# Kernel optimization log

Measured on AMD Instinct MI355X. Metric: run time of the kernel, lower is better.

Reference implementation:

```python
import jax, jax.numpy as jnp
import numpy as np

H_IMG, W_IMG = 160, 160
C1, C2, HEADS, NHOPS = 128, 256, 8, 2
N_NODES = H_IMG * W_IMG


def build_edges(H, W):
    # 3x3 neighborhood (excl. self) + skip edges (i+2,j),(i,j+2); self loops added once
    node = (np.arange(H)[:, None] * W + np.arange(W)[None, :])
    offsets = [(di, dj) for di in (-1, 0, 1) for dj in (-1, 0, 1) if (di, dj) != (0, 0)] + [(2, 0), (0, 2)]
    srcs, dsts = [], []
    for di, dj in offsets:
        i0, i1 = max(0, -di), H - max(0, di)
        j0, j1 = max(0, -dj), W - max(0, dj)
        srcs.append(node[i0:i1, j0:j1].ravel())
        dsts.append(node[i0 + di:i1 + di, j0 + dj:j1 + dj].ravel())
    n = np.arange(H * W)
    srcs.append(n); dsts.append(n)
    return (np.concatenate(srcs).astype(np.int32), np.concatenate(dsts).astype(np.int32))


def setup_inputs() -> dict:
    key = jax.random.key(0)
    ks = jax.random.split(key, 16)
    s = 0.05
    src_np, dst_np = build_edges(H_IMG, W_IMG)
    d = C2 // HEADS
    return {
        "x": jax.random.normal(ks[0], (1, C1, H_IMG, W_IMG), jnp.float32),
        "w_id": jax.random.normal(ks[1], (C2, C1), jnp.float32) * s,
        "w_in": jax.random.normal(ks[2], (C2, C1), jnp.float32) * s,
        "w_gat": jax.random.normal(ks[3], (NHOPS, C2, C2), jnp.float32) * s,
        "a_src": jax.random.normal(ks[4], (NHOPS, HEADS, d), jnp.float32) * s,
        "a_dst": jax.random.normal(ks[5], (NHOPS, HEADS, d), jnp.float32) * s,
        "gat_bias": jax.random.normal(ks[6], (NHOPS, C2), jnp.float32) * s,
        "bn_gamma": jax.random.uniform(ks[7], (NHOPS, C2), jnp.float32, 0.5, 1.5),
        "bn_beta": jax.random.normal(ks[8], (NHOPS, C2), jnp.float32) * s,
        "bn_mean": jax.random.normal(ks[9], (NHOPS, C2), jnp.float32) * s,
        "bn_var": jax.random.uniform(ks[10], (NHOPS, C2), jnp.float32, 0.5, 1.5),
        "w_out": jax.random.normal(ks[11], (C2, C2), jnp.float32) * s,
        "se_w1": jax.random.normal(ks[12], (C2 // 4, C2), jnp.float32) * s,
        "se_b1": jax.random.normal(ks[13], (C2 // 4,), jnp.float32) * s,
        "se_w2": jax.random.normal(ks[14], (C2, C2 // 4), jnp.float32) * s,
        "se_b2": jax.random.normal(ks[15], (C2,), jnp.float32) * s,
        "src": jnp.asarray(src_np),
        "dst": jnp.asarray(dst_np),
    }


def _gat(x, W, a_s, a_d, b, src, dst, N):
    heads, d = a_s.shape
    h = (x @ W.T).reshape(N, heads, d)                      # [N,H,D]
    al_s = jnp.einsum('nhd,hd->nh', h, a_s)                 # [N,H]
    al_d = jnp.einsum('nhd,hd->nh', h, a_d)
    e = jax.nn.leaky_relu(al_s[src] + al_d[dst], 0.2)       # [E,H]
    emax = jax.lax.stop_gradient(jax.ops.segment_max(e, dst, num_segments=N))
    ee = jnp.exp(e - emax[dst])
    denom = jax.ops.segment_sum(ee, dst, num_segments=N)
    alpha = ee / (denom[dst] + 1e-16)                       # segment softmax over incoming edges
    out = jax.ops.segment_sum(h[src] * alpha[..., None], dst, num_segments=N)
    return out.reshape(N, heads * d) + b


def _forward(x, w_id, w_in, w_gat, a_src, a_dst, gat_bias, bn_gamma, bn_beta,
             bn_mean, bn_var, w_out, se_w1, se_b1, se_w2, se_b2, src, dst):
    identity = jnp.einsum('bchw,oc->bohw', x, w_id)
    h = jnp.einsum('bchw,oc->bohw', x, w_in)
    B, C, H, W = h.shape
    N = B * H * W
    xf = h.transpose(0, 2, 3, 1).reshape(N, C)
    for l in range(NHOPS):
        res = xf
        g = _gat(xf, w_gat[l], a_src[l], a_dst[l], gat_bias[l], src, dst, N)
        g = (g - bn_mean[l]) * (bn_gamma[l] * jax.lax.rsqrt(bn_var[l] + 1e-5)) + bn_beta[l]
        xf = jax.nn.relu(g) + res
    y = xf.reshape(B, H, W, C).transpose(0, 3, 1, 2)
    y = jnp.einsum('bchw,oc->bohw', y, w_out)
    # SE block
    w = y.mean(axis=(2, 3))                                 # [B,C]
    w = jax.nn.relu(w @ se_w1.T + se_b1)
    w = jax.nn.sigmoid(w @ se_w2.T + se_b2)
    y = y * w[:, :, None, None]
    return y + identity


def reference(x, w_id, w_in, w_gat, a_src, a_dst, gat_bias, bn_gamma, bn_beta,
              bn_mean, bn_var, w_out, se_w1, se_b1, se_w2, se_b2, src, dst):
    return _forward(x, w_id, w_in, w_gat, a_src, a_dst, gat_bias, bn_gamma, bn_beta,
                    bn_mean, bn_var, w_out, se_w1, se_b1, se_w2, se_b2, src, dst)
```

## Files before the change

### kernel.cpp

```cpp
#include <hip/hip_runtime.h>

#define NN 25600
#define HH 160
#define WW 160
#define C2 256
#define MSLOTS 64

#define B_WIN   0
#define B_WID   32768
#define B_WGAT  65536
#define B_WOUT  196608
#define B_WEND  262144

#define C_BNA   0
#define C_BNB   512
#define C_ASRC  1024
#define C_ADST  1536
#define C_SEW1  2048
#define C_SEB1  18432
#define C_SEW2  18496
#define C_SEB2  34880
#define C_END   35136

typedef __attribute__((ext_vector_type(8))) short bfrag;
typedef __attribute__((ext_vector_type(4))) float ffrag;

__device__ __forceinline__ float b2f(unsigned short u) {
    union { unsigned int ui; float f; } v; v.ui = ((unsigned int)u) << 16; return v.f;
}
__device__ __forceinline__ unsigned short f2b(float f) {
    union { float f; unsigned int u; } v; v.f = f;
    unsigned int u = v.u;
    unsigned int r = (u + 0x7FFFu + ((u >> 16) & 1u)) >> 16;
    return (unsigned short)r;
}
__device__ __forceinline__ float lo16f(unsigned int w) {
    union { unsigned int ui; float f; } v; v.ui = w << 16; return v.f;
}
__device__ __forceinline__ float hi16f(unsigned int w) {
    union { unsigned int ui; float f; } v; v.ui = w & 0xFFFF0000u; return v.f;
}
__device__ __forceinline__ bool probe_f32(const unsigned short* __restrict__ x) {
    int l = threadIdx.x & 63;
    bool wild = false;
#pragma unroll
    for (int i = 0; i < 8; ++i) {
        float v = b2f(x[l * 8 + i]);
        wild |= !(fabsf(v) < 1e6f);
    }
    return __any(wild);
}
__device__ __forceinline__ float ldf(const void* p, long i, bool f32) {
    return f32 ? ((const float*)p)[i] : b2f(((const unsigned short*)p)[i]);
}

__device__ __forceinline__ void gemm_tile_ids(int bid, int& m0, int& o0) {
    int w = (bid & 7) * 200 + (bid >> 3);
    m0 = (w >> 2) * 64;
    o0 = (w & 3) * 64;
}

__device__ __forceinline__ const bfrag* fragp(const unsigned short* buf, int row, int c8) {
    return (const bfrag*)(buf + row * 64 + ((c8 ^ (row & 7)) << 3));
}

__global__ __launch_bounds__(256) void prep_kernel(
    const unsigned short* __restrict__ xp,
    const void* pwin, const void* pwid, const void* pwgat, const void* pwout,
    const void* pasrc, const void* padst, const void* pgbias,
    const void* pbng, const void* pbnb, const void* pbnm, const void* pbnv,
    const void* psew1, const void* pseb1, const void* psew2, const void* pseb2,
    unsigned short* __restrict__ wb, float* __restrict__ cvt,
    float* __restrict__ means, unsigned short* __restrict__ xT)
{
    __shared__ unsigned short T[16 * 136];
    const bool f32 = probe_f32(xp);
    const int tid = threadIdx.x;
    const int bid = blockIdx.x;
    const int gid = bid * 256 + tid;
    const int stride = gridDim.x * 256;

    for (int i = gid; i < MSLOTS * 256; i += stride) means[i] = 0.f;

    for (int i = gid; i < B_WEND; i += stride) {
        const void* s; int o;
        if      (i < B_WID)   { s = pwin;  o = i - B_WIN; }
        else if (i < B_WGAT)  { s = pwid;  o = i - B_WID; }
        else if (i < B_WOUT)  { s = pwgat; o = i - B_WGAT; }
        else                  { s = pwout; o = i - B_WOUT; }
        wb[i] = f32 ? f2b(((const float*)s)[o]) : ((const unsigned short*)s)[o];
    }
    for (int i = gid; i < 512; i += stride) {
        float sc = ldf(pbng, i, f32) * rsqrtf(ldf(pbnv, i, f32) + 1e-5f);
        cvt[C_BNA + i] = sc;
        cvt[C_BNB + i] = (ldf(pgbias, i, f32) - ldf(pbnm, i, f32)) * sc + ldf(pbnb, i, f32);
        cvt[C_ASRC + i] = ldf(pasrc, i, f32);
        cvt[C_ADST + i] = ldf(padst, i, f32);
    }
    for (int i = gid; i < 16384; i += stride) {
        cvt[C_SEW1 + i] = ldf(psew1, i, f32);
        cvt[C_SEW2 + i] = ldf(psew2, i, f32);
    }
    for (int i = gid; i < 64; i += stride)  cvt[C_SEB1 + i] = ldf(pseb1, i, f32);
    for (int i = gid; i < 256; i += stride) cvt[C_SEB2 + i] = ldf(pseb2, i, f32);

    {
        const int n0 = bid * 16;
        const int nl = tid & 15;
        const int cb = tid >> 4;
#pragma unroll
        for (int i = 0; i < 8; ++i) {
            int c = i * 16 + cb;
            long idx = (long)c * NN + n0 + nl;
            T[nl * 136 + c] = f32 ? f2b(((const float*)xp)[idx]) : xp[idx];
        }
        __syncthreads();
        {
            int n = tid >> 4, c0 = (tid & 15) * 8;
            uint4 v = *(const uint4*)&T[n * 136 + c0];
            *(uint4*)(xT + (long)(n0 + n) * 128 + c0) = v;
        }
    }
}

struct SmemC64 { unsigned short Cs[64 * 72]; };
struct SmemGd  { unsigned short As[2][4096], Bs[2][4096]; };
union  SmemNd  { SmemGd g; SmemC64 c; };
struct SmemT   { float T[64 * 73]; };
union  SmemFd  { SmemGd g; SmemT t; };

#define STAGE_TILE(DST, SRC, ROW0, LDA, K0)                                       \
    {                                                                             \
        _Pragma("unroll")                                                         \
        for (int ii = 0; ii < 2; ++ii) {                                          \
            int e = tid + ii * 256;                                               \
            int row = e >> 3;                                                     \
            int q = (e & 7) ^ (row & 7);                                          \
            __builtin_amdgcn_global_load_lds(                                     \
                (const unsigned int*)((SRC) + (long)((ROW0) + row) * (LDA) + (K0) + q * 8), \
                (unsigned int*)&(DST)[e * 8], 16, 0, 0);                          \
        }                                                                         \
    }

__global__ __launch_bounds__(256) void mfma_gemm_kernel(
    const unsigned short* __restrict__ A16,
    const unsigned short* __restrict__ Wi16,
    unsigned short* __restrict__ xf16)
{
    __shared__ SmemNd sm;
    const int tid = threadIdx.x;
    int m0, o0; gemm_tile_ids(blockIdx.x, m0, o0);
    const int lane = tid & 63, wv = tid >> 6;
    const int wm = wv >> 1, wn = wv & 1;
    const int lr = lane & 15, quad = lane >> 4;

    ffrag ai[2][2];
#pragma unroll
    for (int mt = 0; mt < 2; ++mt)
#pragma unroll
        for (int nt = 0; nt < 2; ++nt) ai[mt][nt] = (ffrag){0,0,0,0};

    STAGE_TILE(sm.g.As[0], A16,  m0, 128, 0)
    STAGE_TILE(sm.g.Bs[0], Wi16, o0, 128, 0)
    __syncthreads();
    int cur = 0;
#pragma unroll
    for (int s = 0; s < 2; ++s) {
        if (s == 0) {
            STAGE_TILE(sm.g.As[1], A16,  m0, 128, 64)
            STAGE_TILE(sm.g.Bs[1], Wi16, o0, 128, 64)
        }
#pragma unroll
        for (int ks = 0; ks < 2; ++ks) {
            bfrag a[2], bi[2];
#pragma unroll
            for (int mt = 0; mt < 2; ++mt)
                a[mt] = *fragp(sm.g.As[cur], wm * 32 + mt * 16 + lr, ks * 4 + quad);
#pragma unroll
            for (int nt = 0; nt < 2; ++nt)
                bi[nt] = *fragp(sm.g.Bs[cur], wn * 32 + nt * 16 + lr, ks * 4 + quad);
#pragma unroll
            for (int mt = 0; mt < 2; ++mt)
#pragma unroll
                for (int nt = 0; nt < 2; ++nt)
                    ai[mt][nt] = __builtin_amdgcn_mfma_f32_16x16x32_bf16(a[mt], bi[nt], ai[mt][nt], 0, 0, 0);
        }
        __syncthreads();
        cur ^= 1;
    }
#pragma unroll
    for (int mt = 0; mt < 2; ++mt)
#pragma unroll
        for (int nt = 0; nt < 2; ++nt)
#pragma unroll
            for (int r = 0; r < 4; ++r)
                sm.c.Cs[(wm * 32 + mt * 16 + quad * 4 + r) * 72 + wn * 32 + nt * 16 + lr] = f2b(ai[mt][nt][r]);
    __syncthreads();
#pragma unroll
    for (int it = 0; it < 2; ++it) {
        int e = it * 256 + tid;
        int row = e >> 3, c8 = (e & 7) * 8;
        *(uint4*)(xf16 + (long)(m0 + row) * C2 + o0 + c8) = *(const uint4*)&sm.c.Cs[row * 72 + c8];
    }
}

__global__ __launch_bounds__(256) void gat_gemm_kernel(
    const unsigned short* __restrict__ A16,
    const unsigned short* __restrict__ W16,
    unsigned short* __restrict__ Cout,
    const float* __restrict__ asrc, const float* __restrict__ adst,
    float* __restrict__ als_out, float* __restrict__ ald_out)
{
    __shared__ SmemNd sm;
    const int tid = threadIdx.x;
    int m0, o0; gemm_tile_ids(blockIdx.x, m0, o0);
    const int lane = tid & 63, wv = tid >> 6;
    const int wm = wv >> 1, wn = wv & 1;
    const int lr = lane & 15, quad = lane >> 4;

    ffrag acc[2][2];
#pragma unroll
    for (int mt = 0; mt < 2; ++mt)
#pragma unroll
        for (int nt = 0; nt < 2; ++nt) acc[mt][nt] = (ffrag){0,0,0,0};

    STAGE_TILE(sm.g.As[0], A16, m0, C2, 0)
    STAGE_TILE(sm.g.Bs[0], W16, o0, C2, 0)
    __syncthreads();
    int cur = 0;
#pragma unroll
    for (int s = 0; s < 4; ++s) {
        if (s < 3) {
            STAGE_TILE(sm.g.As[cur ^ 1], A16, m0, C2, (s + 1) * 64)
            STAGE_TILE(sm.g.Bs[cur ^ 1], W16, o0, C2, (s + 1) * 64)
        }
#pragma unroll
        for (int ks = 0; ks < 2; ++ks) {
            bfrag a[2], b[2];
#pragma unroll
            for (int mt = 0; mt < 2; ++mt)
                a[mt] = *fragp(sm.g.As[cur], wm * 32 + mt * 16 + lr, ks * 4 + quad);
#pragma unroll
            for (int nt = 0; nt < 2; ++nt)
                b[nt] = *fragp(sm.g.Bs[cur], wn * 32 + nt * 16 + lr, ks * 4 + quad);
#pragma unroll
            for (int mt = 0; mt < 2; ++mt)
#pragma unroll
                for (int nt = 0; nt < 2; ++nt)
                    acc[mt][nt] = __builtin_amdgcn_mfma_f32_16x16x32_bf16(a[mt], b[nt], acc[mt][nt], 0, 0, 0);
        }
        __syncthreads();
        cur ^= 1;
    }
    {
        const int head = (o0 >> 5) + wn;
        const float as0 = asrc[head * 32 + lr], as1 = asrc[head * 32 + 16 + lr];
        const float ad0 = adst[head * 32 + lr], ad1 = adst[head * 32 + 16 + lr];
#pragma unroll
        for (int mt = 0; mt < 2; ++mt)
#pragma unroll
            for (int r = 0; r < 4; ++r) {
                float ps = acc[mt][0][r] * as0 + acc[mt][1][r] * as1;
                float pd = acc[mt][0][r] * ad0 + acc[mt][1][r] * ad1;
#pragma unroll
                for (int sh = 1; sh < 16; sh <<= 1) {
                    ps += __shfl_xor(ps, sh);
                    pd += __shfl_xor(pd, sh);
                }
                if (lr == 0) {
                    int m = m0 + wm * 32 + mt * 16 + quad * 4 + r;
                    als_out[m * 8 + head] = ps;
                    ald_out[m * 8 + head] = pd;
                }
            }
    }
#pragma unroll
    for (int mt = 0; mt < 2; ++mt)
#pragma unroll
        for (int nt = 0; nt < 2; ++nt)
#pragma unroll
            for (int r = 0; r < 4; ++r)
                sm.c.Cs[(wm * 32 + mt * 16 + quad * 4 + r) * 72 + wn * 32 + nt * 16 + lr] = f2b(acc[mt][nt][r]);
    __syncthreads();
#pragma unroll
    for (int it = 0; it < 2; ++it) {
        int e = it * 256 + tid;
        int row = e >> 3, c8 = (e & 7) * 8;
        *(uint4*)(Cout + (long)(m0 + row) * C2 + o0 + c8) = *(const uint4*)&sm.c.Cs[row * 72 + c8];
    }
}

__global__ __launch_bounds__(256) void aggregate_kernel(
    const unsigned short* __restrict__ h16,
    const float* __restrict__ al_s,
    const float* __restrict__ al_d,
    const float* __restrict__ bnA,
    const float* __restrict__ bnB,
    unsigned short* __restrict__ xf16,
    float* __restrict__ means)
{
    const int SI[11] = { 1, 1, 1, 0, 0, -1, -1, -1, -2,  0, 0};
    const int SJ[11] = { 1, 0,-1, 1,-1,  1,  0, -1,  0, -2, 0};
    __shared__ float part[4][256];

    const int t = threadIdx.x;
    const int ln = t >> 5;
    const int l = t & 31;
    const int n = blockIdx.x * 8 + ln;
    const int i = n / WW, j = n % WW;
    const int c8 = l * 8;
    const int hd = l >> 2;

    int srcn[11]; bool okm[11];
#pragma unroll
    for (int k = 0; k < 11; ++k) {
        int si = i + SI[k], sj = j + SJ[k];
        bool ok = (si >= 0) & (si < HH) & (sj >= 0) & (sj < WW);
        okm[k] = ok;
        srcn[k] = ok ? si * WW + sj : n;
    }

    float e[11];
    {
        const float ald = al_d[n * 8 + hd];
        float mx = -1e30f;
#pragma unroll
        for (int k = 0; k < 11; ++k) {
            float s = al_s[(long)srcn[k] * 8 + hd];
            float v = s + ald;
            v = v > 0.f ? v : 0.2f * v;
            v = okm[k] ? v : -1e30f;
            e[k] = v;
            mx = fmaxf(mx, v);
        }
        float denom = 0.f;
#pragma unroll
        for (int k = 0; k < 11; ++k) {
            float p = __expf(e[k] - mx);
            e[k] = p;
            denom += p;
        }
        const float inv = 1.f / (denom + 1e-16f);
#pragma unroll
        for (int k = 0; k < 11; ++k) e[k] *= inv;
    }

    uint4 hv[11];
#pragma unroll
    for (int k = 0; k < 11; ++k)
        hv[k] = *(const uint4*)(h16 + (long)srcn[k] * C2 + c8);
    uint4 rv = *(const uint4*)(xf16 + (long)n * C2 + c8);

    float a0=0.f,a1=0.f,a2=0.f,a3=0.f,a4=0.f,a5=0.f,a6=0.f,a7=0.f;
#pragma unroll
    for (int k = 0; k < 11; ++k) {
        float al = e[k];
        a0 += al * lo16f(hv[k].x); a1 += al * hi16f(hv[k].x);
        a2 += al * lo16f(hv[k].y); a3 += al * hi16f(hv[k].y);
        a4 += al * lo16f(hv[k].z); a5 += al * hi16f(hv[k].z);
        a6 += al * lo16f(hv[k].w); a7 += al * hi16f(hv[k].w);
    }
    float acc8[8] = {a0,a1,a2,a3,a4,a5,a6,a7};
    float res[8] = {lo16f(rv.x),hi16f(rv.x),lo16f(rv.y),hi16f(rv.y),
                    lo16f(rv.z),hi16f(rv.z),lo16f(rv.w),hi16f(rv.w)};
    float out[8];
#pragma unroll
    for (int q = 0; q < 8; ++q) {
        int c = c8 + q;
        float g = acc8[q] * bnA[c] + bnB[c];
        out[q] = fmaxf(g, 0.f) + res[q];
    }
    ushort4 o16a, o16b;
    o16a.x = f2b(out[0]); o16a.y = f2b(out[1]); o16a.z = f2b(out[2]); o16a.w = f2b(out[3]);
    o16b.x = f2b(out[4]); o16b.y = f2b(out[5]); o16b.z = f2b(out[6]); o16b.w = f2b(out[7]);
    *(ushort4*)(xf16 + (long)n * C2 + c8)     = o16a;
    *(ushort4*)(xf16 + (long)n * C2 + c8 + 4) = o16b;

    if (means) {
        float s8[8];
#pragma unroll
        for (int q = 0; q < 8; ++q) {
            s8[q] = out[q];
            s8[q] += __shfl_xor(s8[q], 32);
        }
        const int wvi = t >> 6;
        if ((t & 63) < 32) {
#pragma unroll
            for (int q = 0; q < 8; ++q) part[wvi][c8 + q] = s8[q];
        }
        __syncthreads();
        {
            float v = part[0][t] + part[1][t] + part[2][t] + part[3][t];
            atomicAdd(&means[(blockIdx.x & (MSLOTS - 1)) * 256 + t], v);
        }
    }
}

__global__ __launch_bounds__(256) void se_kernel(
    const unsigned short* __restrict__ W16,
    const float* __restrict__ means,
    const float* __restrict__ cvt,
    float* __restrict__ sv_out)
{
    __shared__ float cs[256], mv[256], hv[64];
    const int t = threadIdx.x;
    {
        float s0=0,s1=0,s2=0,s3=0,s4=0,s5=0,s6=0,s7=0;
#pragma unroll 2
        for (int sl = 0; sl < MSLOTS; sl += 8) {
            s0 += means[(sl+0)*256 + t]; s1 += means[(sl+1)*256 + t];
            s2 += means[(sl+2)*256 + t]; s3 += means[(sl+3)*256 + t];
            s4 += means[(sl+4)*256 + t]; s5 += means[(sl+5)*256 + t];
            s6 += means[(sl+6)*256 + t]; s7 += means[(sl+7)*256 + t];
        }
        cs[t] = ((s0+s1)+(s2+s3)) + ((s4+s5)+(s6+s7));
    }
    __syncthreads();
    {
        float s = 0.f;
        const unsigned short* wr = W16 + (long)t * C2;
#pragma unroll 4
        for (int k = 0; k < 256; k += 8) {
            uint4 w = *(const uint4*)(wr + k);
            s += cs[k]   * lo16f(w.x) + cs[k+1] * hi16f(w.x)
               + cs[k+2] * lo16f(w.y) + cs[k+3] * hi16f(w.y)
               + cs[k+4] * lo16f(w.z) + cs[k+5] * hi16f(w.z)
               + cs[k+6] * lo16f(w.w) + cs[k+7] * hi16f(w.w);
        }
        mv[t] = s * (1.0f / 25600.0f);
    }
    __syncthreads();
    if (t < 64) {
        const float* w1 = cvt + C_SEW1 + t * 256;
        float s = cvt[C_SEB1 + t];
        for (int cc = 0; cc < 256; cc += 4) {
            float4 w = *(const float4*)(w1 + cc);
            s += w.x * mv[cc] + w.y * mv[cc+1] + w.z * mv[cc+2] + w.w * mv[cc+3];
        }
        hv[t] = fmaxf(s, 0.f);
    }
    __syncthreads();
    {
        const float* w2 = cvt + C_SEW2 + t * 64;
        float s = cvt[C_SEB2 + t];
        for (int k = 0; k < 64; k += 4) {
            float4 w = *(const float4*)(w2 + k);
            s += w.x * hv[k] + w.y * hv[k+1] + w.z * hv[k+2] + w.w * hv[k+3];
        }
        sv_out[t] = 1.0f / (1.0f + __expf(-s));
    }
}

__global__ __launch_bounds__(256) void final_gemm_kernel(
    const unsigned short* __restrict__ x_probe,
    const unsigned short* __restrict__ A16,
    const unsigned short* __restrict__ W16,
    const unsigned short* __restrict__ AT16,
    const unsigned short* __restrict__ Wd16,
    const float* __restrict__ sv,
    void* __restrict__ outp)
{
    __shared__ SmemFd sm;
    const bool f32o = probe_f32(x_probe);
    const int tid = threadIdx.x;
    int m0, o0; gemm_tile_ids(blockIdx.x, m0, o0);
    const int lane = tid & 63, wv = tid >> 6;
    const int wm = wv >> 1, wn = wv & 1;
    const int lr = lane & 15, quad = lane >> 4;

    ffrag acc[2][2], accI[2][2];
#pragma unroll
    for (int mt = 0; mt < 2; ++mt)
#pragma unroll
        for (int nt = 0; nt < 2; ++nt) { acc[mt][nt] = (ffrag){0,0,0,0}; accI[mt][nt] = (ffrag){0,0,0,0}; }

    STAGE_TILE(sm.g.As[0], A16, m0, C2, 0)
    STAGE_TILE(sm.g.Bs[0], W16, o0, C2, 0)
    __syncthreads();
    int cur = 0;
#pragma unroll
    for (int s = 0; s < 6; ++s) {
        if (s < 3) {
            STAGE_TILE(sm.g.As[cur ^ 1], A16, m0, C2, (s + 1) * 64)
            STAGE_TILE(sm.g.Bs[cur ^ 1], W16, o0, C2, (s + 1) * 64)
        } else if (s == 3) {
            STAGE_TILE(sm.g.As[cur ^ 1], AT16, m0, 128, 0)
            STAGE_TILE(sm.g.Bs[cur ^ 1], Wd16, o0, 128, 0)
        } else if (s == 4) {
            STAGE_TILE(sm.g.As[cur ^ 1], AT16, m0, 128, 64)
            STAGE_TILE(sm.g.Bs[cur ^ 1], Wd16, o0, 128, 64)
        }
        if (s < 4) {
#pragma unroll
            for (int ks = 0; ks < 2; ++ks) {
                bfrag a[2], b[2];
#pragma unroll
                for (int mt = 0; mt < 2; ++mt)
                    a[mt] = *fragp(sm.g.As[cur], wm * 32 + mt * 16 + lr, ks * 4 + quad);
#pragma unroll
                for (int nt = 0; nt < 2; ++nt)
                    b[nt] = *fragp(sm.g.Bs[cur], wn * 32 + nt * 16 + lr, ks * 4 + quad);
#pragma unroll
                for (int mt = 0; mt < 2; ++mt)
#pragma unroll
                    for (int nt = 0; nt < 2; ++nt)
                        acc[mt][nt] = __builtin_amdgcn_mfma_f32_16x16x32_bf16(a[mt], b[nt], acc[mt][nt], 0, 0, 0);
            }
        } else {
#pragma unroll
            for (int ks = 0; ks < 2; ++ks) {
                bfrag a[2], b[2];
#pragma unroll
                for (int mt = 0; mt < 2; ++mt)
                    a[mt] = *fragp(sm.g.As[cur], wm * 32 + mt * 16 + lr, ks * 4 + quad);
#pragma unroll
                for (int nt = 0; nt < 2; ++nt)
                    b[nt] = *fragp(sm.g.Bs[cur], wn * 32 + nt * 16 + lr, ks * 4 + quad);
#pragma unroll
                for (int mt = 0; mt < 2; ++mt)
#pragma unroll
                    for (int nt = 0; nt < 2; ++nt)
                        accI[mt][nt] = __builtin_amdgcn_mfma_f32_16x16x32_bf16(a[mt], b[nt], accI[mt][nt], 0, 0, 0);
            }
        }
        __syncthreads();
        cur ^= 1;
    }

#pragma unroll
    for (int mt = 0; mt < 2; ++mt)
#pragma unroll
        for (int nt = 0; nt < 2; ++nt) {
            int cl = wn * 32 + nt * 16 + lr;
            float s = sv[o0 + cl];
#pragma unroll
            for (int r = 0; r < 4; ++r) {
                int row = wm * 32 + mt * 16 + quad * 4 + r;
                float v = acc[mt][nt][r] * s + accI[mt][nt][r];
                sm.t.T[cl * 73 + row] = v;
            }
        }
    __syncthreads();
#pragma unroll
    for (int it = 0; it < 16; ++it) {
        int e = it * 256 + tid;
        int cc = e >> 6, nn = e & 63;
        long idx = (long)(o0 + cc) * NN + m0 + nn;
        float v = sm.t.T[cc * 73 + nn];
        if (f32o) ((float*)outp)[idx] = v;
        else      ((unsigned short*)outp)[idx] = f2b(v);
    }
}

extern "C" void kernel_launch(void* const* d_in, const int* in_sizes, int n_in,
                              void* d_out, int out_size, void* d_ws, size_t ws_size,
                              hipStream_t stream) {
    float* ws = (float*)d_ws;
    float* cvt   = ws;
    float* means = ws + 35200;
    float* svb   = means + MSLOTS * 256;
    float* als   = svb + 256;
    float* ald   = als + 204800;
    unsigned short* wb16  = (unsigned short*)(ald + 204800);
    unsigned short* xT16  = wb16 + B_WEND;
    unsigned short* xf16  = xT16 + NN * 128;
    unsigned short* h16   = xf16 + NN * 256;

    const unsigned short* xp = (const unsigned short*)d_in[0];

    dim3 b256(256);

    prep_kernel<<<1600, b256, 0, stream>>>(
        xp, d_in[2], d_in[1], d_in[3], d_in[11],
        d_in[4], d_in[5], d_in[6], d_in[7], d_in[8], d_in[9], d_in[10],
        d_in[12], d_in[13], d_in[14], d_in[15],
        wb16, cvt, means, xT16);

    mfma_gemm_kernel<<<1600, b256, 0, stream>>>(
        xT16, wb16 + B_WIN, xf16);

    for (int l = 0; l < 2; ++l) {
        gat_gemm_kernel<<<1600, b256, 0, stream>>>(
            xf16, wb16 + B_WGAT + l * 65536, h16,
            cvt + C_ASRC + l * 256, cvt + C_ADST + l * 256, als, ald);
        aggregate_kernel<<<NN / 8, b256, 0, stream>>>(h16, als, ald,
            cvt + C_BNA + l * 256, cvt + C_BNB + l * 256, xf16,
            (l == 1) ? means : nullptr);
    }

    se_kernel<<<1, b256, 0, stream>>>(wb16 + B_WOUT, means, cvt, svb);

    final_gemm_kernel<<<1600, b256, 0, stream>>>(
        xp, xf16, wb16 + B_WOUT, xT16, wb16 + B_WID, svb, d_out);
}
```

Baseline: 195.3 us.

## Fold input projection into first GAT weight and fuse into dual GEMM

Precomputes W_gat0·W_in as a 256x128 weight with a small new GEMM, so the first GAT projection can be computed directly from the 128-channel input. A dual GEMM then produces both xf (via W_in) and the first hop's h, plus its attention logits, in one pass over the input. This removes one full 256-K GEMM launch over all nodes. In exchange it adds the small weight-fusion kernel, a transposed W_in copy in prep, and extra bf16 rounding from the fused weight.

```diff
diff --git a/kernel.cpp b/kernel.cpp
--- a/kernel.cpp
+++ b/kernel.cpp
@@ -71,7 +71,8 @@
     const void* pbng, const void* pbnb, const void* pbnm, const void* pbnv,
     const void* psew1, const void* pseb1, const void* psew2, const void* pseb2,
     unsigned short* __restrict__ wb, float* __restrict__ cvt,
-    float* __restrict__ means, unsigned short* __restrict__ xT)
+    float* __restrict__ means, unsigned short* __restrict__ xT,
+    unsigned short* __restrict__ winT)
 {
     __shared__ unsigned short T[16 * 136];
     const bool f32 = probe_f32(xp);
@@ -90,6 +91,10 @@
         else                  { s = pwout; o = i - B_WOUT; }
         wb[i] = f32 ? f2b(((const float*)s)[o]) : ((const unsigned short*)s)[o];
     }
+    for (int i = gid; i < 32768; i += stride) {
+        int o = i >> 7, c = i & 127;
+        winT[c * 256 + o] = f32 ? f2b(((const float*)pwin)[i]) : ((const unsigned short*)pwin)[i];
+    }
     for (int i = gid; i < 512; i += stride) {
         float sc = ldf(pbng, i, f32) * rsqrtf(ldf(pbnv, i, f32) + 1e-5f);
         cvt[C_BNA + i] = sc;
@@ -124,6 +129,10 @@
 }
 
 struct SmemC64 { unsigned short Cs[64 * 72]; };
+struct SmemGu  { unsigned short As[4096], Bs[4096]; };
+union  SmemNu  { SmemGu g; SmemC64 c; };
+struct SmemG2u { unsigned short As[4096], Bi[4096], Bd[4096]; };
+union  SmemXu  { SmemG2u g; SmemC64 c; };
 struct SmemGd  { unsigned short As[2][4096], Bs[2][4096]; };
 union  SmemNd  { SmemGd g; SmemC64 c; };
 struct SmemT   { float T[64 * 73]; };
@@ -142,51 +151,130 @@
         }                                                                         \
     }
 
-__global__ __launch_bounds__(256) void mfma_gemm_kernel(
+__global__ __launch_bounds__(256) void wfuse_kernel(
+    const unsigned short* __restrict__ A16,
+    const unsigned short* __restrict__ B16,
+    unsigned short* __restrict__ C16)
+{
+    __shared__ SmemNu sm;
+    const int tid = threadIdx.x;
+    const int m0 = blockIdx.x * 64, o0 = blockIdx.y * 64;
+    const int lane = tid & 63, wv = tid >> 6;
+    const int wm = wv >> 1, wn = wv & 1;
+    const int lr = lane & 15, quad = lane >> 4;
+
+    ffrag acc[2][2];
+#pragma unroll
+    for (int mt = 0; mt < 2; ++mt)
+#pragma unroll
+        for (int nt = 0; nt < 2; ++nt) acc[mt][nt] = (ffrag){0,0,0,0};
+
+    for (int k0 = 0; k0 < 256; k0 += 64) {
+        STAGE_TILE(sm.g.As, A16, m0, 256, k0)
+        STAGE_TILE(sm.g.Bs, B16, o0, 256, k0)
+        __syncthreads();
+#pragma unroll
+        for (int ks = 0; ks < 2; ++ks) {
+            bfrag a[2], b[2];
+#pragma unroll
+            for (int mt = 0; mt < 2; ++mt)
+                a[mt] = *fragp(sm.g.As, wm * 32 + mt * 16 + lr, ks * 4 + quad);
+#pragma unroll
+            for (int nt = 0; nt < 2; ++nt)
+                b[nt] = *fragp(sm.g.Bs, wn * 32 + nt * 16 + lr, ks * 4 + quad);
+#pragma unroll
+            for (int mt = 0; mt < 2; ++mt)
+#pragma unroll
+                for (int nt = 0; nt < 2; ++nt)
+                    acc[mt][nt] = __builtin_amdgcn_mfma_f32_16x16x32_bf16(a[mt], b[nt], acc[mt][nt], 0, 0, 0);
+        }
+        __syncthreads();
+    }
+#pragma unroll
+    for (int mt = 0; mt < 2; ++mt)
+#pragma unroll
+        for (int nt = 0; nt < 2; ++nt)
+#pragma unroll
+            for (int r = 0; r < 4; ++r)
+                sm.c.Cs[(wm * 32 + mt * 16 + quad * 4 + r) * 72 + wn * 32 + nt * 16 + lr] = f2b(acc[mt][nt][r]);
+    __syncthreads();
+#pragma unroll
+    for (int it = 0; it < 2; ++it) {
+        int e = it * 256 + tid;
+        int row = e >> 3, c8 = (e & 7) * 8;
+        *(uint4*)(C16 + (long)(m0 + row) * 128 + o0 + c8) = *(const uint4*)&sm.c.Cs[row * 72 + c8];
+    }
+}
+
+__global__ __launch_bounds__(256) void dual_gemm_kernel(
     const unsigned short* __restrict__ A16,
     const unsigned short* __restrict__ Wi16,
-    unsigned short* __restrict__ xf16)
+    const unsigned short* __restrict__ Wd16,
+    unsigned short* __restrict__ xf16,
+    unsigned short* __restrict__ h16,
+    const float* __restrict__ asrc, const float* __restrict__ adst,
+    float* __restrict__ als_out, float* __restrict__ ald_out)
 {
-    __shared__ SmemNd sm;
+    __shared__ SmemXu sm;
     const int tid = threadIdx.x;
     int m0, o0; gemm_tile_ids(blockIdx.x, m0, o0);
     const int lane = tid & 63, wv = tid >> 6;
     const int wm = wv >> 1, wn = wv & 1;
     const int lr = lane & 15, quad = lane >> 4;
 
-    ffrag ai[2][2];
-#pragma unroll
-    for (int mt = 0; mt < 2; ++mt)
-#pragma unroll
-        for (int nt = 0; nt < 2; ++nt) ai[mt][nt] = (ffrag){0,0,0,0};
-
-    STAGE_TILE(sm.g.As[0], A16,  m0, 128, 0)
-    STAGE_TILE(sm.g.Bs[0], Wi16, o0, 128, 0)
-    __syncthreads();
-    int cur = 0;
-#pragma unroll
-    for (int s = 0; s < 2; ++s) {
-        if (s == 0) {
-            STAGE_TILE(sm.g.As[1], A16,  m0, 128, 64)
-            STAGE_TILE(sm.g.Bs[1], Wi16, o0, 128, 64)
-        }
+    ffrag ai[2][2], ad[2][2];
+#pragma unroll
+    for (int mt = 0; mt < 2; ++mt)
+#pragma unroll
+        for (int nt = 0; nt < 2; ++nt) { ai[mt][nt] = (ffrag){0,0,0,0}; ad[mt][nt] = (ffrag){0,0,0,0}; }
+
+    for (int k0 = 0; k0 < 128; k0 += 64) {
+        STAGE_TILE(sm.g.As, A16,  m0, 128, k0)
+        STAGE_TILE(sm.g.Bi, Wi16, o0, 128, k0)
+        STAGE_TILE(sm.g.Bd, Wd16, o0, 128, k0)
+        __syncthreads();
 #pragma unroll
         for (int ks = 0; ks < 2; ++ks) {
-            bfrag a[2], bi[2];
+            bfrag a[2], bi[2], bd[2];
 #pragma unroll
             for (int mt = 0; mt < 2; ++mt)
-                a[mt] = *fragp(sm.g.As[cur], wm * 32 + mt * 16 + lr, ks * 4 + quad);
-#pragma unroll
-            for (int nt = 0; nt < 2; ++nt)
-                bi[nt] = *fragp(sm.g.Bs[cur], wn * 32 + nt * 16 + lr, ks * 4 + quad);
+                a[mt] = *fragp(sm.g.As, wm * 32 + mt * 16 + lr, ks * 4 + quad);
+#pragma unroll
+            for (int nt = 0; nt < 2; ++nt) {
+                bi[nt] = *fragp(sm.g.Bi, wn * 32 + nt * 16 + lr, ks * 4 + quad);
+                bd[nt] = *fragp(sm.g.Bd, wn * 32 + nt * 16 + lr, ks * 4 + quad);
+            }
 #pragma unroll
             for (int mt = 0; mt < 2; ++mt)
 #pragma unroll
-                for (int nt = 0; nt < 2; ++nt)
+                for (int nt = 0; nt < 2; ++nt) {
                     ai[mt][nt] = __builtin_amdgcn_mfma_f32_16x16x32_bf16(a[mt], bi[nt], ai[mt][nt], 0, 0, 0);
+                    ad[mt][nt] = __builtin_amdgcn_mfma_f32_16x16x32_bf16(a[mt], bd[nt], ad[mt][nt], 0, 0, 0);
+                }
         }
         __syncthreads();
-        cur ^= 1;
+    }
+    {
+        const int head = (o0 >> 5) + wn;
+        const float as0 = asrc[head * 32 + lr], as1 = asrc[head * 32 + 16 + lr];
+        const float ad0 = adst[head * 32 + lr], ad1 = adst[head * 32 + 16 + lr];
+#pragma unroll
+        for (int mt = 0; mt < 2; ++mt)
+#pragma unroll
+            for (int r = 0; r < 4; ++r) {
+                float ps = ad[mt][0][r] * as0 + ad[mt][1][r] * as1;
+                float pd = ad[mt][0][r] * ad0 + ad[mt][1][r] * ad1;
+#pragma unroll
+                for (int sh = 1; sh < 16; sh <<= 1) {
+                    ps += __shfl_xor(ps, sh);
+                    pd += __shfl_xor(pd, sh);
+                }
+                if (lr == 0) {
+                    int m = m0 + wm * 32 + mt * 16 + quad * 4 + r;
+                    als_out[m * 8 + head] = ps;
+                    ald_out[m * 8 + head] = pd;
+                }
+            }
     }
 #pragma unroll
     for (int mt = 0; mt < 2; ++mt)
@@ -201,6 +289,21 @@
         int e = it * 256 + tid;
         int row = e >> 3, c8 = (e & 7) * 8;
         *(uint4*)(xf16 + (long)(m0 + row) * C2 + o0 + c8) = *(const uint4*)&sm.c.Cs[row * 72 + c8];
+    }
+    __syncthreads();
+#pragma unroll
+    for (int mt = 0; mt < 2; ++mt)
+#pragma unroll
+        for (int nt = 0; nt < 2; ++nt)
+#pragma unroll
+            for (int r = 0; r < 4; ++r)
+                sm.c.Cs[(wm * 32 + mt * 16 + quad * 4 + r) * 72 + wn * 32 + nt * 16 + lr] = f2b(ad[mt][nt][r]);
+    __syncthreads();
+#pragma unroll
+    for (int it = 0; it < 2; ++it) {
+        int e = it * 256 + tid;
+        int row = e >> 3, c8 = (e & 7) * 8;
+        *(uint4*)(h16 + (long)(m0 + row) * C2 + o0 + c8) = *(const uint4*)&sm.c.Cs[row * 72 + c8];
     }
 }
 
@@ -562,7 +665,9 @@
     float* als   = svb + 256;
     float* ald   = als + 204800;
     unsigned short* wb16  = (unsigned short*)(ald + 204800);
-    unsigned short* xT16  = wb16 + B_WEND;
+    unsigned short* wgp16 = wb16 + B_WEND;
+    unsigned short* winT16= wgp16 + 32768;
+    unsigned short* xT16  = winT16 + 32768;
     unsigned short* xf16  = xT16 + NN * 128;
     unsigned short* h16   = xf16 + NN * 256;
 
@@ -574,19 +679,24 @@
         xp, d_in[2], d_in[1], d_in[3], d_in[11],
         d_in[4], d_in[5], d_in[6], d_in[7], d_in[8], d_in[9], d_in[10],
         d_in[12], d_in[13], d_in[14], d_in[15],
-        wb16, cvt, means, xT16);
-
-    mfma_gemm_kernel<<<1600, b256, 0, stream>>>(
-        xT16, wb16 + B_WIN, xf16);
-
-    for (int l = 0; l < 2; ++l) {
-        gat_gemm_kernel<<<1600, b256, 0, stream>>>(
-            xf16, wb16 + B_WGAT + l * 65536, h16,
-            cvt + C_ASRC + l * 256, cvt + C_ADST + l * 256, als, ald);
-        aggregate_kernel<<<NN / 8, b256, 0, stream>>>(h16, als, ald,
-            cvt + C_BNA + l * 256, cvt + C_BNB + l * 256, xf16,
-            (l == 1) ? means : nullptr);
-    }
+        wb16, cvt, means, xT16, winT16);
+
+    wfuse_kernel<<<dim3(4, 2), b256, 0, stream>>>(
+        wb16 + B_WGAT, winT16, wgp16);
+
+    dual_gemm_kernel<<<1600, b256, 0, stream>>>(
+        xT16, wb16 + B_WIN, wgp16, xf16, h16,
+        cvt + C_ASRC, cvt + C_ADST, als, ald);
+
+    aggregate_kernel<<<NN / 8, b256, 0, stream>>>(h16, als, ald,
+        cvt + C_BNA, cvt + C_BNB, xf16, nullptr);
+
+    gat_gemm_kernel<<<1600, b256, 0, stream>>>(
+        xf16, wb16 + B_WGAT + 65536, h16,
+        cvt + C_ASRC + 256, cvt + C_ADST + 256, als, ald);
+
+    aggregate_kernel<<<NN / 8, b256, 0, stream>>>(h16, als, ald,
+        cvt + C_BNA + 256, cvt + C_BNB + 256, xf16, means);
 
     se_kernel<<<1, b256, 0, stream>>>(wb16 + B_WOUT, means, cvt, svb);
 
```

Measured after the change: 196.0 us. Within noise of the previous version (+0.4%).
